# Optimization experiments

Measured on AMD Instinct MI355X. Metric: run time of the kernel, lower is better.

## Reference

```python
import jax, jax.numpy as jnp
import numpy as np

E = 1024
H = 16
DFF = 4 * E
EPS = 1e-5


def layer_norm(x, scale, bias):
    mu = jnp.mean(x, axis=-1, keepdims=True)
    var = jnp.var(x, axis=-1, keepdims=True)
    return (x - mu) * jax.lax.rsqrt(var + EPS) * scale + bias


def setup_inputs() -> dict:
    key = jax.random.key(0)
    ks = jax.random.split(key, 12)
    N, L = 2, 2048
    x = jax.random.normal(ks[0], (N, L, E), dtype=jnp.float32)
    attn_mask = jax.random.randint(ks[1], (N, H, L, L), 0, 2) == 1
    s = 0.02
    return {
        "x": x,
        "attn_mask": attn_mask,
        "ln1_s": jnp.ones((E,), jnp.float32),
        "ln1_b": jnp.zeros((E,), jnp.float32),
        "Wqkv": jax.random.normal(ks[2], (E, 3 * E), jnp.float32) * s,
        "bqkv": jnp.zeros((3 * E,), jnp.float32),
        "Wo": jax.random.normal(ks[3], (E, E), jnp.float32) * s,
        "bo": jnp.zeros((E,), jnp.float32),
        "ln2_s": jnp.ones((E,), jnp.float32),
        "ln2_b": jnp.zeros((E,), jnp.float32),
        "lnf_s": jnp.ones((E,), jnp.float32),
        "lnf_b": jnp.zeros((E,), jnp.float32),
        "W1": jax.random.normal(ks[4], (E, DFF), jnp.float32) * s,
        "b1": jnp.zeros((DFF,), jnp.float32),
        "W2": jax.random.normal(ks[5], (DFF, E), jnp.float32) * s,
        "b2": jnp.zeros((E,), jnp.float32),
    }


def reference(x, attn_mask, ln1_s, ln1_b, Wqkv, bqkv, Wo, bo,
              ln2_s, ln2_b, lnf_s, lnf_b, W1, b1, W2, b2):
    N, L, _ = x.shape
    D = E // H
    # --- self attention (pre-norm) ---
    h = layer_norm(x, ln1_s, ln1_b)
    qkv = h @ Wqkv + bqkv                      # [N,L,3E]
    q, k, v = jnp.split(qkv, 3, axis=-1)
    q = q.reshape(N, L, H, D)
    k = k.reshape(N, L, H, D)
    v = v.reshape(N, L, H, D)
    a = jnp.einsum('nqhd,nkhd->nhqk', q, k) * (D ** -0.5)  # [N,H,L,L]
    a = jnp.where(attn_mask, -jnp.inf, a)
    a = jax.nn.softmax(a, axis=-1)
    o = jnp.einsum('nhqk,nkhd->nqhd', a, v).reshape(N, L, E)
    o = o @ Wo + bo
    x = x + o
    # --- feedforward (norm_2 then FF's internal LN) ---
    h = layer_norm(x, ln2_s, ln2_b)
    h = layer_norm(h, lnf_s, lnf_b)
    h = jax.nn.gelu(h @ W1 + b1, approximate=False) @ W2 + b2
    return x + h
```

## Files before the change

### kernel.cpp

```cpp
#include <hip/hip_runtime.h>
#include <math.h>

#define E_DIM 1024
#define H_HEADS 16
#define D_HEAD 64
#define DFF_DIM 4096
#define L_SEQ 2048
#define N_BATCH 2
#define T_TOK (N_BATCH * L_SEQ)

typedef __attribute__((ext_vector_type(8))) __bf16 bf16x8;
typedef __attribute__((ext_vector_type(4))) float f32x4;

__device__ __forceinline__ unsigned short f2bf(float f) {
  union { float f; unsigned int u; } v; v.f = f;
  unsigned int r = v.u + 0x7fffu + ((v.u >> 16) & 1u);
  return (unsigned short)(r >> 16);
}

__device__ __forceinline__ void gld16(const void* g, void* l) {
  __builtin_amdgcn_global_load_lds(
      (const __attribute__((address_space(1))) unsigned int*)g,
      (__attribute__((address_space(3))) unsigned int*)l, 16, 0, 0);
}

__global__ __launch_bounds__(256) void convert_transpose(
    const float* __restrict__ in, unsigned short* __restrict__ out, int K, int N) {
  __shared__ float tile[32][33];
  int n0 = blockIdx.x * 32, k0 = blockIdx.y * 32;
  int tx = threadIdx.x & 31, ty = threadIdx.x >> 5;
#pragma unroll
  for (int i = 0; i < 32; i += 8)
    tile[ty + i][tx] = in[(size_t)(k0 + ty + i) * N + n0 + tx];
  __syncthreads();
#pragma unroll
  for (int i = 0; i < 32; i += 8)
    out[(size_t)(n0 + ty + i) * K + k0 + tx] = f2bf(tile[tx][ty + i]);
}

__device__ __forceinline__ void block_reduce2(float& a, float& b, float* sm, int tid) {
#pragma unroll
  for (int off = 32; off > 0; off >>= 1) {
    a += __shfl_down(a, off);
    b += __shfl_down(b, off);
  }
  int wid = tid >> 6;
  if ((tid & 63) == 0) { sm[wid * 2] = a; sm[wid * 2 + 1] = b; }
  __syncthreads();
  a = sm[0] + sm[2] + sm[4] + sm[6];
  b = sm[1] + sm[3] + sm[5] + sm[7];
}

__global__ __launch_bounds__(256) void ln_kernel(
    const float* __restrict__ x, const float* __restrict__ s,
    const float* __restrict__ b, unsigned short* __restrict__ out) {
  int row = blockIdx.x, tid = threadIdx.x;
  __shared__ float sm[8];
  float4 v = ((const float4*)(x + (size_t)row * E_DIM))[tid];
  float sum = v.x + v.y + v.z + v.w;
  float sq = v.x * v.x + v.y * v.y + v.z * v.z + v.w * v.w;
  block_reduce2(sum, sq, sm, tid);
  float mu = sum * (1.0f / E_DIM);
  float var = sq * (1.0f / E_DIM) - mu * mu;
  float rs = rsqrtf(var + 1e-5f);
  float4 sv = ((const float4*)s)[tid];
  float4 bv = ((const float4*)b)[tid];
  ushort4 o4;
  o4.x = f2bf((v.x - mu) * rs * sv.x + bv.x);
  o4.y = f2bf((v.y - mu) * rs * sv.y + bv.y);
  o4.z = f2bf((v.z - mu) * rs * sv.z + bv.z);
  o4.w = f2bf((v.w - mu) * rs * sv.w + bv.w);
  ((ushort4*)(out + (size_t)row * E_DIM))[tid] = o4;
}

__global__ __launch_bounds__(256) void ln2_fused_kernel(
    const float* __restrict__ p0, const float* __restrict__ p1,
    const float* __restrict__ x, const float* __restrict__ bo,
    const float* __restrict__ s2, const float* __restrict__ b2,
    const float* __restrict__ sf, const float* __restrict__ bf_,
    float* __restrict__ x2, unsigned short* __restrict__ out) {
  int row = blockIdx.x, tid = threadIdx.x;
  __shared__ float sm[8];
  float4 a0 = ((const float4*)(p0 + (size_t)row * E_DIM))[tid];
  float4 a1 = ((const float4*)(p1 + (size_t)row * E_DIM))[tid];
  float4 xv = ((const float4*)(x + (size_t)row * E_DIM))[tid];
  float4 bov = ((const float4*)bo)[tid];
  float4 v;
  v.x = a0.x + a1.x + xv.x + bov.x;
  v.y = a0.y + a1.y + xv.y + bov.y;
  v.z = a0.z + a1.z + xv.z + bov.z;
  v.w = a0.w + a1.w + xv.w + bov.w;
  ((float4*)(x2 + (size_t)row * E_DIM))[tid] = v;
  float sum = v.x + v.y + v.z + v.w;
  float sq = v.x * v.x + v.y * v.y + v.z * v.z + v.w * v.w;
  block_reduce2(sum, sq, sm, tid);
  float mu = sum * (1.0f / E_DIM);
  float rs = rsqrtf(sq * (1.0f / E_DIM) - mu * mu + 1e-5f);
  float4 s2v = ((const float4*)s2)[tid];
  float4 b2v = ((const float4*)b2)[tid];
  float y0 = (v.x - mu) * rs * s2v.x + b2v.x;
  float y1 = (v.y - mu) * rs * s2v.y + b2v.y;
  float y2 = (v.z - mu) * rs * s2v.z + b2v.z;
  float y3 = (v.w - mu) * rs * s2v.w + b2v.w;
  float sum2 = y0 + y1 + y2 + y3;
  float sq2 = y0 * y0 + y1 * y1 + y2 * y2 + y3 * y3;
  __syncthreads();
  block_reduce2(sum2, sq2, sm, tid);
  float mu2 = sum2 * (1.0f / E_DIM);
  float rs2 = rsqrtf(sq2 * (1.0f / E_DIM) - mu2 * mu2 + 1e-5f);
  float4 sfv = ((const float4*)sf)[tid];
  float4 bfv = ((const float4*)bf_)[tid];
  ushort4 o4;
  o4.x = f2bf((y0 - mu2) * rs2 * sfv.x + bfv.x);
  o4.y = f2bf((y1 - mu2) * rs2 * sfv.y + bfv.y);
  o4.z = f2bf((y2 - mu2) * rs2 * sfv.z + bfv.z);
  o4.w = f2bf((y3 - mu2) * rs2 * sfv.w + bfv.w);
  ((ushort4*)(out + (size_t)row * E_DIM))[tid] = o4;
}

__global__ __launch_bounds__(256) void add4_kernel(
    const float* __restrict__ p0, const float* __restrict__ p1,
    const float* __restrict__ p2, const float* __restrict__ p3,
    const float* __restrict__ resid, const float* __restrict__ bias,
    float* __restrict__ out) {
  int row = blockIdx.x, tid = threadIdx.x;
  size_t base = (size_t)row * E_DIM;
  float4 a0 = ((const float4*)(p0 + base))[tid];
  float4 a1 = ((const float4*)(p1 + base))[tid];
  float4 a2 = ((const float4*)(p2 + base))[tid];
  float4 a3 = ((const float4*)(p3 + base))[tid];
  float4 rv = ((const float4*)(resid + base))[tid];
  float4 bv = ((const float4*)bias)[tid];
  float4 o;
  o.x = a0.x + a1.x + a2.x + a3.x + rv.x + bv.x;
  o.y = a0.y + a1.y + a2.y + a3.y + rv.y + bv.y;
  o.z = a0.z + a1.z + a2.z + a3.z + rv.z + bv.z;
  o.w = a0.w + a1.w + a2.w + a3.w + rv.w + bv.w;
  ((float4*)(out + base))[tid] = o;
}

template <int EPI>
__global__ __launch_bounds__(256) void gemm_bt(
    const unsigned short* __restrict__ A, const unsigned short* __restrict__ Bt,
    const float* __restrict__ bias, void* __restrict__ outp,
    int M, int N, int K, int Ks) {
  __shared__ unsigned short As[128 * 32];
  __shared__ unsigned short Bs[128 * 32];
  int tid = threadIdx.x;
  int lane = tid & 63, wave = tid >> 6;
  int m0 = blockIdx.y * 128, n0 = blockIdx.x * 128;
  int kz = blockIdx.z * Ks;
  int wm = (wave & 1) * 64, wn = (wave >> 1) * 64;
  int lm = lane & 15, lq = lane >> 4;
  int srow = wave * 32 + (lane >> 2);
  int scol = (lane & 3) * 8;
  const unsigned short* Ag = A + (size_t)(m0 + srow) * K + scol;
  const unsigned short* Bg = Bt + (size_t)(n0 + srow) * K + scol;
  unsigned short* AsW = As + wave * 1024;
  unsigned short* BsW = Bs + wave * 1024;
  f32x4 acc[4][4] = {};
  for (int k0 = kz; k0 < kz + Ks; k0 += 32) {
    __syncthreads();
    gld16(Ag + k0, AsW);
    gld16(Ag + (size_t)16 * K + k0, AsW + 512);
    gld16(Bg + k0, BsW);
    gld16(Bg + (size_t)16 * K + k0, BsW + 512);
    __syncthreads();
    bf16x8 a[4], b[4];
#pragma unroll
    for (int i = 0; i < 4; i++)
      a[i] = *(const bf16x8*)(As + (wm + i * 16 + lm) * 32 + lq * 8);
#pragma unroll
    for (int j = 0; j < 4; j++)
      b[j] = *(const bf16x8*)(Bs + (wn + j * 16 + lm) * 32 + lq * 8);
#pragma unroll
    for (int i = 0; i < 4; i++)
#pragma unroll
      for (int j = 0; j < 4; j++)
        acc[i][j] = __builtin_amdgcn_mfma_f32_16x16x32_bf16(a[i], b[j], acc[i][j], 0, 0, 0);
  }
  float* pout = (EPI == 3) ? ((float*)outp + (size_t)blockIdx.z * M * N) : nullptr;
#pragma unroll
  for (int i = 0; i < 4; i++)
#pragma unroll
    for (int j = 0; j < 4; j++) {
      int row = m0 + wm + i * 16 + lq * 4;
      int col = n0 + wn + j * 16 + lm;
      float bcol = (EPI == 3) ? 0.0f : bias[col];
#pragma unroll
      for (int r = 0; r < 4; r++) {
        float v = acc[i][j][r] + bcol;
        size_t idx = (size_t)(row + r) * N + col;
        if (EPI == 0) {
          ((unsigned short*)outp)[idx] = f2bf(v);
        } else if (EPI == 1) {
          float g = 0.5f * v * (1.0f + erff(v * 0.70710678118f));
          ((unsigned short*)outp)[idx] = f2bf(g);
        } else {
          pout[idx] = v;
        }
      }
    }
}

__global__ __launch_bounds__(256) void attn_kernel(
    const unsigned short* __restrict__ qkv, const int* __restrict__ mask,
    unsigned short* __restrict__ o) {
  const int bq = blockIdx.x;
  const int nh = blockIdx.y;
  const int h = nh & 15;
  const int tid = threadIdx.x, lane = tid & 63, wave = tid >> 6;
  const int lm = lane & 15, lq = lane >> 4;

  __shared__ unsigned short Ksm[2][64 * 72];
  __shared__ unsigned short Vtm[2][64 * 72];
  __shared__ unsigned short Ps[4][16 * 72];

  const int q_base = bq * 64;
  const int tok0 = (nh >> 4) * L_SEQ;
  const int qoff = h * 64, koff = E_DIM + h * 64, voff = 2 * E_DIM + h * 64;
  const int* mbase = mask + (size_t)nh * L_SEQ * L_SEQ;

  bf16x8 qf[2];
  {
    int t = tok0 + q_base + wave * 16 + lm;
    const unsigned short* qr = qkv + (size_t)t * (3 * E_DIM) + qoff + lq * 8;
    qf[0] = *(const bf16x8*)(qr);
    qf[1] = *(const bf16x8*)(qr + 32);
  }

  const int qrow = q_base + wave * 16 + lq * 4;
  const int srow = tid >> 3, schunk = tid & 7;
  const size_t TS = 3 * E_DIM;
  const unsigned short* kg = qkv + (size_t)(tok0 + srow) * TS + koff + schunk * 8;
  const unsigned short* vg = qkv + (size_t)(tok0 + srow) * TS + voff + schunk * 8;

  uint4 kreg[2], vreg[2];
  int mreg[16];

  auto load_kv = [&](int kt) {
#pragma unroll
    for (int it = 0; it < 2; it++) {
      size_t toff = (size_t)(kt * 64 + it * 32) * TS;
      kreg[it] = *(const uint4*)(kg + toff);
      vreg[it] = *(const uint4*)(vg + toff);
    }
  };
  auto load_m = [&](int kt) {
#pragma unroll
    for (int nt = 0; nt < 4; nt++)
#pragma unroll
      for (int r = 0; r < 4; r++)
        mreg[nt * 4 + r] =
            mbase[(size_t)(qrow + r) * L_SEQ + kt * 64 + nt * 16 + lm];
  };
  auto store_kv = [&](int buf) {
#pragma unroll
    for (int it = 0; it < 2; it++) {
      int key = srow + it * 32;
      *(uint4*)(Ksm[buf] + key * 72 + schunk * 8) = kreg[it];
      const unsigned short* vs = (const unsigned short*)&vreg[it];
      int kcol = key ^ (schunk << 3);
#pragma unroll
      for (int jj = 0; jj < 8; jj++)
        Vtm[buf][(schunk * 8 + jj) * 72 + kcol] = vs[jj];
    }
  };

  float m_run[4], l_run[4];
  f32x4 oacc[4] = {};
#pragma unroll
  for (int r = 0; r < 4; r++) { m_run[r] = -1e30f; l_run[r] = 0.0f; }

  load_kv(0);
  load_m(0);
  store_kv(0);
  __syncthreads();

  int cur = 0;
  const int NT = L_SEQ / 64;
  for (int kt = 0; kt < NT; kt++) {
    f32x4 s[4];
    __builtin_amdgcn_s_setprio(1);
#pragma unroll
    for (int nt = 0; nt < 4; nt++) {
      bf16x8 kb0 = *(const bf16x8*)(Ksm[cur] + (nt * 16 + lm) * 72 + lq * 8);
      bf16x8 kb1 = *(const bf16x8*)(Ksm[cur] + (nt * 16 + lm) * 72 + 32 + lq * 8);
      f32x4 acc = {};
      acc = __builtin_amdgcn_mfma_f32_16x16x32_bf16(qf[0], kb0, acc, 0, 0, 0);
      acc = __builtin_amdgcn_mfma_f32_16x16x32_bf16(qf[1], kb1, acc, 0, 0, 0);
      s[nt] = acc;
    }
    __builtin_amdgcn_s_setprio(0);

#pragma unroll
    for (int nt = 0; nt < 4; nt++)
#pragma unroll
      for (int r = 0; r < 4; r++) {
        float v = s[nt][r] * 0.125f;
        s[nt][r] = mreg[nt * 4 + r] ? -1e30f : v;
      }

    int ktn = (kt + 1 < NT) ? kt + 1 : kt;
    load_kv(ktn);
    load_m(ktn);

    float alpha[4], rsum[4];
#pragma unroll
    for (int r = 0; r < 4; r++) {
      float v = fmaxf(fmaxf(s[0][r], s[1][r]), fmaxf(s[2][r], s[3][r]));
#pragma unroll
      for (int mo = 1; mo < 16; mo <<= 1) v = fmaxf(v, __shfl_xor(v, mo));
      float mn = fmaxf(m_run[r], v);
      alpha[r] = __expf(m_run[r] - mn);
      m_run[r] = mn;
      rsum[r] = 0.0f;
    }
    unsigned short* pw = Ps[wave];
#pragma unroll
    for (int nt = 0; nt < 4; nt++)
#pragma unroll
      for (int r = 0; r < 4; r++) {
        float p = __expf(s[nt][r] - m_run[r]);
        rsum[r] += p;
        pw[(lq * 4 + r) * 72 + nt * 16 + lm] = f2bf(p);
      }
#pragma unroll
    for (int r = 0; r < 4; r++) {
      float v = rsum[r];
#pragma unroll
      for (int mo = 1; mo < 16; mo <<= 1) v += __shfl_xor(v, mo);
      l_run[r] = l_run[r] * alpha[r] + v;
    }
#pragma unroll
    for (int j = 0; j < 4; j++)
#pragma unroll
      for (int r = 0; r < 4; r++) oacc[j][r] *= alpha[r];

    asm volatile("s_waitcnt lgkmcnt(0)" ::: "memory");
    __builtin_amdgcn_sched_barrier(0);

    __builtin_amdgcn_s_setprio(1);
#pragma unroll
    for (int c = 0; c < 2; c++) {
      bf16x8 pa = *(const bf16x8*)(pw + lm * 72 + c * 32 + lq * 8);
#pragma unroll
      for (int j = 0; j < 4; j++) {
        int d = j * 16 + lm;
        int kblk = (c * 4 + lq) ^ ((d >> 3) & 7);
        bf16x8 vb = *(const bf16x8*)(Vtm[cur] + d * 72 + kblk * 8);
        oacc[j] = __builtin_amdgcn_mfma_f32_16x16x32_bf16(pa, vb, oacc[j], 0, 0, 0);
      }
    }
    __builtin_amdgcn_s_setprio(0);

    store_kv(cur ^ 1);
    __syncthreads();
    cur ^= 1;
  }

#pragma unroll
  for (int r = 0; r < 4; r++) {
    float inv_l = 1.0f / l_run[r];
    int t = tok0 + qrow + r;
#pragma unroll
    for (int j = 0; j < 4; j++)
      o[(size_t)t * E_DIM + h * 64 + j * 16 + lm] = f2bf(oacc[j][r] * inv_l);
  }
}

extern "C" void kernel_launch(void* const* d_in, const int* in_sizes, int n_in,
                              void* d_out, int out_size, void* d_ws, size_t ws_size,
                              hipStream_t stream) {
  const float* x = (const float*)d_in[0];
  const int* mask = (const int*)d_in[1];
  const float* ln1_s = (const float*)d_in[2];
  const float* ln1_b = (const float*)d_in[3];
  const float* Wqkv = (const float*)d_in[4];
  const float* bqkv = (const float*)d_in[5];
  const float* Wo = (const float*)d_in[6];
  const float* bo = (const float*)d_in[7];
  const float* ln2_s = (const float*)d_in[8];
  const float* ln2_b = (const float*)d_in[9];
  const float* lnf_s = (const float*)d_in[10];
  const float* lnf_b = (const float*)d_in[11];
  const float* W1 = (const float*)d_in[12];
  const float* b1 = (const float*)d_in[13];
  const float* W2 = (const float*)d_in[14];
  const float* b2 = (const float*)d_in[15];

  size_t off = 0;
  auto alloc = [&](size_t bytes) {
    void* p = (char*)d_ws + off;
    off += (bytes + 255) & ~(size_t)255;
    return p;
  };
  unsigned short* WqkvT = (unsigned short*)alloc((size_t)3072 * 1024 * 2);
  unsigned short* WoT = (unsigned short*)alloc((size_t)1024 * 1024 * 2);
  unsigned short* W1T = (unsigned short*)alloc((size_t)4096 * 1024 * 2);
  unsigned short* W2T = (unsigned short*)alloc((size_t)1024 * 4096 * 2);
  unsigned short* h1 = (unsigned short*)alloc((size_t)T_TOK * E_DIM * 2);
  unsigned short* qkvb = (unsigned short*)alloc((size_t)T_TOK * 3 * E_DIM * 2);
  unsigned short* ob = (unsigned short*)alloc((size_t)T_TOK * E_DIM * 2);
  float* x2 = (float*)alloc((size_t)T_TOK * E_DIM * 4);
  unsigned short* h2 = (unsigned short*)alloc((size_t)T_TOK * E_DIM * 2);
  unsigned short* g1 = (unsigned short*)alloc((size_t)T_TOK * DFF_DIM * 2);
  float* part = (float*)alloc((size_t)4 * T_TOK * E_DIM * 4);
  const size_t PSTRIDE = (size_t)T_TOK * E_DIM;

  convert_transpose<<<dim3(3072 / 32, 1024 / 32), 256, 0, stream>>>(Wqkv, WqkvT, 1024, 3072);
  convert_transpose<<<dim3(1024 / 32, 1024 / 32), 256, 0, stream>>>(Wo, WoT, 1024, 1024);
  convert_transpose<<<dim3(4096 / 32, 1024 / 32), 256, 0, stream>>>(W1, W1T, 1024, 4096);
  convert_transpose<<<dim3(1024 / 32, 4096 / 32), 256, 0, stream>>>(W2, W2T, 4096, 1024);
  ln_kernel<<<T_TOK, 256, 0, stream>>>(x, ln1_s, ln1_b, h1);
  gemm_bt<0><<<dim3(3072 / 128, T_TOK / 128, 1), 256, 0, stream>>>(
      h1, WqkvT, bqkv, qkvb, T_TOK, 3072, 1024, 1024);
  attn_kernel<<<dim3(L_SEQ / 64, N_BATCH * H_HEADS), 256, 0, stream>>>(qkvb, mask, ob);
  gemm_bt<3><<<dim3(1024 / 128, T_TOK / 128, 2), 256, 0, stream>>>(
      ob, WoT, nullptr, part, T_TOK, 1024, 1024, 512);
  ln2_fused_kernel<<<T_TOK, 256, 0, stream>>>(
      part, part + PSTRIDE, x, bo, ln2_s, ln2_b, lnf_s, lnf_b, x2, h2);
  gemm_bt<1><<<dim3(DFF_DIM / 128, T_TOK / 128, 1), 256, 0, stream>>>(
      h2, W1T, b1, g1, T_TOK, DFF_DIM, 1024, 1024);
  gemm_bt<3><<<dim3(1024 / 128, T_TOK / 128, 4), 256, 0, stream>>>(
      g1, W2T, nullptr, part, T_TOK, 1024, 4096, 1024);
  add4_kernel<<<T_TOK, 256, 0, stream>>>(
      part, part + PSTRIDE, part + 2 * PSTRIDE, part + 3 * PSTRIDE,
      x2, b2, (float*)d_out);

  (void)in_sizes; (void)n_in; (void)out_size; (void)ws_size;
}
```

Measured before the change: 1.060 ms.

## Pre-transpose V globally and stage K/V via direct global-to-LDS loads

Adds a separate kernel that writes V transposed per head into a workspace buffer. The attention kernel then stages K and V tiles with global_load_lds straight into XOR-swizzled, unpadded LDS buffers, issued at the top of each iteration. This replaces the register round trip and the scalar transposed V stores into LDS. The P buffer also moves to the same swizzle. The cost is an extra kernel launch and an extra read and write of V through HBM.

```diff
diff --git a/kernel.cpp b/kernel.cpp
--- a/kernel.cpp
+++ b/kernel.cpp
@@ -36,6 +36,32 @@
 #pragma unroll
   for (int i = 0; i < 32; i += 8)
     out[(size_t)(n0 + ty + i) * K + k0 + tx] = f2bf(tile[tx][ty + i]);
+}
+
+__global__ __launch_bounds__(256) void v_transpose(
+    const unsigned short* __restrict__ qkv, unsigned short* __restrict__ vtg) {
+  __shared__ unsigned short t[64][72];
+  int kb = blockIdx.x * 64;
+  int nh = blockIdx.y, n = nh >> 4, h = nh & 15;
+  int tid = threadIdx.x;
+  int r = tid >> 3, ch = tid & 7;
+  const size_t TS = 3 * E_DIM;
+  const size_t voff = 2 * E_DIM + h * 64;
+#pragma unroll
+  for (int it = 0; it < 2; it++) {
+    int row = r + it * 32;
+    uint4 v = *(const uint4*)(qkv + (size_t)(n * L_SEQ + kb + row) * TS + voff + ch * 8);
+    *(uint4*)(&t[row][ch * 8]) = v;
+  }
+  __syncthreads();
+#pragma unroll
+  for (int it = 0; it < 2; it++) {
+    int d = r + it * 32;
+    unsigned short tmp[8];
+#pragma unroll
+    for (int s = 0; s < 8; s++) tmp[s] = t[ch * 8 + s][d];
+    *(uint4*)(vtg + ((size_t)nh * 64 + d) * L_SEQ + kb + ch * 8) = *(uint4*)tmp;
+  }
 }
 
 __device__ __forceinline__ void block_reduce2(float& a, float& b, float* sm, int tid) {
@@ -204,48 +230,52 @@
 }
 
 __global__ __launch_bounds__(256) void attn_kernel(
-    const unsigned short* __restrict__ qkv, const int* __restrict__ mask,
+    const unsigned short* __restrict__ qkv,
+    const unsigned short* __restrict__ vtg,
+    const int* __restrict__ mask,
     unsigned short* __restrict__ o) {
   const int bq = blockIdx.x;
   const int nh = blockIdx.y;
   const int h = nh & 15;
   const int tid = threadIdx.x, lane = tid & 63, wave = tid >> 6;
-  const int lm = lane & 15, lq = lane >> 4;
-
-  __shared__ unsigned short Ksm[2][64 * 72];
-  __shared__ unsigned short Vtm[2][64 * 72];
-  __shared__ unsigned short Ps[4][16 * 72];
+  const int lm = lane & 15, lq = lane >> 4, lm7 = lm & 7;
+
+  __shared__ unsigned short Kb[2][64 * 64];
+  __shared__ unsigned short Vb[2][64 * 64];
+  __shared__ unsigned short Ps[4][16 * 64];
 
   const int q_base = bq * 64;
   const int tok0 = (nh >> 4) * L_SEQ;
-  const int qoff = h * 64, koff = E_DIM + h * 64, voff = 2 * E_DIM + h * 64;
+  const int qoff = h * 64, koff = E_DIM + h * 64;
   const int* mbase = mask + (size_t)nh * L_SEQ * L_SEQ;
+  const size_t TS = 3 * E_DIM;
 
   bf16x8 qf[2];
   {
     int t = tok0 + q_base + wave * 16 + lm;
-    const unsigned short* qr = qkv + (size_t)t * (3 * E_DIM) + qoff + lq * 8;
+    const unsigned short* qr = qkv + (size_t)t * TS + qoff + lq * 8;
     qf[0] = *(const bf16x8*)(qr);
     qf[1] = *(const bf16x8*)(qr + 32);
   }
 
   const int qrow = q_base + wave * 16 + lq * 4;
-  const int srow = tid >> 3, schunk = tid & 7;
-  const size_t TS = 3 * E_DIM;
-  const unsigned short* kg = qkv + (size_t)(tok0 + srow) * TS + koff + schunk * 8;
-  const unsigned short* vg = qkv + (size_t)(tok0 + srow) * TS + voff + schunk * 8;
-
-  uint4 kreg[2], vreg[2];
+  const int lrow = lane >> 3;
+  const int xch = ((lane & 7) ^ lrow) * 8;
+  const unsigned short* kgb = qkv + koff + xch;
+  const unsigned short* vgb = vtg + (size_t)nh * 64 * L_SEQ + xch;
+
+  auto STAGE = [&](int buf, int kt) {
+    int kb = kt * 64;
+#pragma unroll
+    for (int cc = 0; cc < 2; cc++) {
+      int c = wave * 2 + cc;
+      int row = c * 8 + lrow;
+      gld16(kgb + (size_t)(tok0 + kb + row) * TS, Kb[buf] + c * 512);
+      gld16(vgb + (size_t)row * L_SEQ + kb, Vb[buf] + c * 512);
+    }
+  };
+
   int mreg[16];
-
-  auto load_kv = [&](int kt) {
-#pragma unroll
-    for (int it = 0; it < 2; it++) {
-      size_t toff = (size_t)(kt * 64 + it * 32) * TS;
-      kreg[it] = *(const uint4*)(kg + toff);
-      vreg[it] = *(const uint4*)(vg + toff);
-    }
-  };
   auto load_m = [&](int kt) {
 #pragma unroll
     for (int nt = 0; nt < 4; nt++)
@@ -254,38 +284,28 @@
         mreg[nt * 4 + r] =
             mbase[(size_t)(qrow + r) * L_SEQ + kt * 64 + nt * 16 + lm];
   };
-  auto store_kv = [&](int buf) {
-#pragma unroll
-    for (int it = 0; it < 2; it++) {
-      int key = srow + it * 32;
-      *(uint4*)(Ksm[buf] + key * 72 + schunk * 8) = kreg[it];
-      const unsigned short* vs = (const unsigned short*)&vreg[it];
-      int kcol = key ^ (schunk << 3);
-#pragma unroll
-      for (int jj = 0; jj < 8; jj++)
-        Vtm[buf][(schunk * 8 + jj) * 72 + kcol] = vs[jj];
-    }
-  };
 
   float m_run[4], l_run[4];
   f32x4 oacc[4] = {};
 #pragma unroll
   for (int r = 0; r < 4; r++) { m_run[r] = -1e30f; l_run[r] = 0.0f; }
 
-  load_kv(0);
+  STAGE(0, 0);
   load_m(0);
-  store_kv(0);
   __syncthreads();
 
   int cur = 0;
   const int NT = L_SEQ / 64;
   for (int kt = 0; kt < NT; kt++) {
+    if (kt + 1 < NT) STAGE(cur ^ 1, kt + 1);
+
     f32x4 s[4];
     __builtin_amdgcn_s_setprio(1);
 #pragma unroll
     for (int nt = 0; nt < 4; nt++) {
-      bf16x8 kb0 = *(const bf16x8*)(Ksm[cur] + (nt * 16 + lm) * 72 + lq * 8);
-      bf16x8 kb1 = *(const bf16x8*)(Ksm[cur] + (nt * 16 + lm) * 72 + 32 + lq * 8);
+      int kidx = (nt * 16 + lm) * 64 + ((lq ^ lm7) << 3);
+      bf16x8 kb0 = *(const bf16x8*)(Kb[cur] + kidx);
+      bf16x8 kb1 = *(const bf16x8*)(Kb[cur] + (kidx ^ 32));
       f32x4 acc = {};
       acc = __builtin_amdgcn_mfma_f32_16x16x32_bf16(qf[0], kb0, acc, 0, 0, 0);
       acc = __builtin_amdgcn_mfma_f32_16x16x32_bf16(qf[1], kb1, acc, 0, 0, 0);
@@ -300,10 +320,7 @@
         float v = s[nt][r] * 0.125f;
         s[nt][r] = mreg[nt * 4 + r] ? -1e30f : v;
       }
-
-    int ktn = (kt + 1 < NT) ? kt + 1 : kt;
-    load_kv(ktn);
-    load_m(ktn);
+    load_m((kt + 1 < NT) ? kt + 1 : kt);
 
     float alpha[4], rsum[4];
 #pragma unroll
@@ -318,13 +335,17 @@
     }
     unsigned short* pw = Ps[wave];
 #pragma unroll
-    for (int nt = 0; nt < 4; nt++)
-#pragma unroll
-      for (int r = 0; r < 4; r++) {
+    for (int r = 0; r < 4; r++) {
+      int prow = lq * 4 + r;
+      int pbase = prow * 64 + lm7;
+      int p7 = prow & 7;
+#pragma unroll
+      for (int nt = 0; nt < 4; nt++) {
         float p = __expf(s[nt][r] - m_run[r]);
         rsum[r] += p;
-        pw[(lq * 4 + r) * 72 + nt * 16 + lm] = f2bf(p);
+        pw[pbase + ((((nt << 1) | (lm >> 3)) ^ p7) << 3)] = f2bf(p);
       }
+    }
 #pragma unroll
     for (int r = 0; r < 4; r++) {
       float v = rsum[r];
@@ -343,18 +364,16 @@
     __builtin_amdgcn_s_setprio(1);
 #pragma unroll
     for (int c = 0; c < 2; c++) {
-      bf16x8 pa = *(const bf16x8*)(pw + lm * 72 + c * 32 + lq * 8);
+      int pc = ((((c << 2) | lq)) ^ lm7) << 3;
+      bf16x8 pa = *(const bf16x8*)(pw + lm * 64 + pc);
 #pragma unroll
       for (int j = 0; j < 4; j++) {
-        int d = j * 16 + lm;
-        int kblk = (c * 4 + lq) ^ ((d >> 3) & 7);
-        bf16x8 vb = *(const bf16x8*)(Vtm[cur] + d * 72 + kblk * 8);
+        bf16x8 vb = *(const bf16x8*)(Vb[cur] + (j * 16 + lm) * 64 + pc);
         oacc[j] = __builtin_amdgcn_mfma_f32_16x16x32_bf16(pa, vb, oacc[j], 0, 0, 0);
       }
     }
     __builtin_amdgcn_s_setprio(0);
 
-    store_kv(cur ^ 1);
     __syncthreads();
     cur ^= 1;
   }
@@ -406,6 +425,7 @@
   unsigned short* h2 = (unsigned short*)alloc((size_t)T_TOK * E_DIM * 2);
   unsigned short* g1 = (unsigned short*)alloc((size_t)T_TOK * DFF_DIM * 2);
   float* part = (float*)alloc((size_t)4 * T_TOK * E_DIM * 4);
+  unsigned short* vtg = (unsigned short*)alloc((size_t)T_TOK * E_DIM * 2);
   const size_t PSTRIDE = (size_t)T_TOK * E_DIM;
 
   convert_transpose<<<dim3(3072 / 32, 1024 / 32), 256, 0, stream>>>(Wqkv, WqkvT, 1024, 3072);
@@ -415,7 +435,9 @@
   ln_kernel<<<T_TOK, 256, 0, stream>>>(x, ln1_s, ln1_b, h1);
   gemm_bt<0><<<dim3(3072 / 128, T_TOK / 128, 1), 256, 0, stream>>>(
       h1, WqkvT, bqkv, qkvb, T_TOK, 3072, 1024, 1024);
-  attn_kernel<<<dim3(L_SEQ / 64, N_BATCH * H_HEADS), 256, 0, stream>>>(qkvb, mask, ob);
+  v_transpose<<<dim3(L_SEQ / 64, N_BATCH * H_HEADS), 256, 0, stream>>>(qkvb, vtg);
+  attn_kernel<<<dim3(L_SEQ / 64, N_BATCH * H_HEADS), 256, 0, stream>>>(
+      qkvb, vtg, mask, ob);
   gemm_bt<3><<<dim3(1024 / 128, T_TOK / 128, 2), 256, 0, stream>>>(
       ob, WoT, nullptr, part, T_TOK, 1024, 1024, 512);
   ln2_fused_kernel<<<T_TOK, 256, 0, stream>>>(
```

Result: no change. 1.072 ms (+1.1%).
